# Performance work log

Hardware: AMD Instinct MI355X
Metric: run time of the kernel (lower is better)

The kernel has to match this reference:

```python
import jax, jax.numpy as jnp
import numpy as np

N_QUBITS = 6
N_QLAYERS = 3
LOGISTIC_R = 3.99
HENON_A, HENON_B = 1.4, 0.3


def _conv1d(x, w, b):
    # x: [B, C_in, T], w: [C_out, C_in, K=3], SAME padding (pad=1)
    y = jax.lax.conv_general_dilated(x, w, window_strides=(1,), padding=((1, 1),),
                                     dimension_numbers=('NCH', 'OIH', 'NCH'))
    return y + b[None, :, None]


def _apply_1q_batched(state, G, q):
    # state: [B,2,...,2], G: [B,2,2] acting on qubit axis 1+q
    s = jnp.moveaxis(state, 1 + q, -1)
    s = jnp.einsum('bij,b...j->b...i', G, s)
    return jnp.moveaxis(s, -1, 1 + q)


def _apply_1q(state, G, q):
    s = jnp.moveaxis(state, 1 + q, -1)
    s = jnp.einsum('ij,b...j->b...i', G, s)
    return jnp.moveaxis(s, -1, 1 + q)


def _apply_cnot(state, c, t):
    s = jnp.moveaxis(state, (1 + c, 1 + t), (-2, -1))
    # control=1 block: flip target amplitudes
    s = jnp.concatenate([s[..., 0:1, :], s[..., 1:2, ::-1]], axis=-2)
    return jnp.moveaxis(s, (-2, -1), (1 + c, 1 + t))


def quantum_expvals(angles, qweights):
    # angles: [B, 6] real encoding angles; qweights: [3, 6] shared RY params
    B = angles.shape[0]
    state = jnp.zeros((B, 2 ** N_QUBITS), jnp.complex64).at[:, 0].set(1.0)
    state = state.reshape((B,) + (2,) * N_QUBITS)
    half = 0.5 * angles
    for i in range(N_QUBITS):
        ax = half[:, i % N_QUBITS]
        ay = half[:, (i + 1) % N_QUBITS]
        az = half[:, (i + 2) % N_QUBITS]
        cx_, sx_ = jnp.cos(ax), jnp.sin(ax)
        RX = jnp.stack([jnp.stack([cx_ + 0j, -1j * sx_], -1),
                        jnp.stack([-1j * sx_, cx_ + 0j], -1)], -2)
        state = _apply_1q_batched(state, RX, i)
        cy_, sy_ = jnp.cos(ay), jnp.sin(ay)
        RY = jnp.stack([jnp.stack([cy_ + 0j, -sy_ + 0j], -1),
                        jnp.stack([sy_ + 0j, cy_ + 0j], -1)], -2)
        state = _apply_1q_batched(state, RY, i)
        ez = jnp.exp(1j * az)
        zero = jnp.zeros_like(ez)
        RZ = jnp.stack([jnp.stack([jnp.conj(ez), zero], -1),
                        jnp.stack([zero, ez], -1)], -2)
        state = _apply_1q_batched(state, RZ, i)
    for l in range(N_QLAYERS):
        for q in range(N_QUBITS):
            a = 0.5 * qweights[l, q]
            c_, s_ = jnp.cos(a), jnp.sin(a)
            RY = jnp.array([[1., 0.], [0., 1.]], jnp.float32) * c_ + \
                 jnp.array([[0., -1.], [1., 0.]], jnp.float32) * s_
            state = _apply_1q(state, RY.astype(jnp.complex64), q)
        for q in range(N_QUBITS):
            state = _apply_cnot(state, q, (q + 1) % N_QUBITS)
    probs = (state * jnp.conj(state)).real  # [B,2,...,2]
    evs = []
    for i in range(N_QUBITS):
        axes = tuple(a for a in range(1, N_QUBITS + 1) if a != 1 + i)
        p = jnp.sum(probs, axis=axes)  # [B,2]
        evs.append(p[:, 0] - p[:, 1])
    return jnp.stack(evs, -1)  # [B,6]


def _lstm_cell(xt, h, c, Wih, Whh, bih, bhh):
    g = xt @ Wih.T + bih + h @ Whh.T + bhh
    i, f, gg, o = jnp.split(g, 4, axis=-1)
    c2 = jax.nn.sigmoid(f) * c + jax.nn.sigmoid(i) * jnp.tanh(gg)
    h2 = jax.nn.sigmoid(o) * jnp.tanh(c2)
    return h2, c2


def _forward(x, w0, b0, w1, b1, w2, b2, Wih, Whh, bih, bhh, qweights, Wfc, bfc, Wout, bout):
    B = x.shape[0]
    t = x.transpose(0, 2, 1)                 # [B, C, T]
    t = jax.nn.relu(_conv1d(t, w0, b0))
    t = jax.nn.relu(_conv1d(t, w1, b1))
    t = jax.nn.relu(_conv1d(t, w2, b2))
    t = t.transpose(2, 0, 1)                 # [T, B, H]
    H = t.shape[2]
    h0 = jnp.zeros((B, H), x.dtype)
    c0 = jnp.zeros((B, H), x.dtype)

    def step(carry, xt):
        h, c = carry
        h, c = _lstm_cell(xt, h, c, Wih, Whh, bih, bhh)
        h = LOGISTIC_R * h * (1.0 - h)
        x0, y0 = h[:, 0], h[:, 1]
        xn = 1.0 - HENON_A * x0 ** 2 + y0
        yn = HENON_B * x0
        h = jnp.concatenate([xn[:, None], yn[:, None], h[:, 2:]], axis=1)
        # QuantumRNNCell called as qrnn(hx, hx): h = h + fc(quantum(h[:, :6]))
        h = h + quantum_expvals(h[:, :N_QUBITS], qweights) @ Wfc.T + bfc
        return (h, c), None

    (h, _), _ = jax.lax.scan(step, (h0, c0), t)
    return jax.nn.sigmoid(h @ Wout.T + bout)  # [B, 1]


def setup_inputs() -> dict:
    key = jax.random.key(0)
    ks = jax.random.split(key, 20)
    B, T, D, Htcn, Hlstm = 1024, 256, 64, 32, 32
    s = 0.1
    inp = {
        'x': jax.random.normal(ks[0], (B, T, D), jnp.float32),
        'w0': jax.random.normal(ks[1], (Htcn, D, 3), jnp.float32) * s,
        'b0': jax.random.normal(ks[2], (Htcn,), jnp.float32) * s,
        'w1': jax.random.normal(ks[3], (Htcn, Htcn, 3), jnp.float32) * s,
        'b1': jax.random.normal(ks[4], (Htcn,), jnp.float32) * s,
        'w2': jax.random.normal(ks[5], (Htcn, Htcn, 3), jnp.float32) * s,
        'b2': jax.random.normal(ks[6], (Htcn,), jnp.float32) * s,
        'Wih': jax.random.normal(ks[7], (4 * Hlstm, Htcn), jnp.float32) * s,
        'Whh': jax.random.normal(ks[8], (4 * Hlstm, Hlstm), jnp.float32) * s,
        'bih': jax.random.normal(ks[9], (4 * Hlstm,), jnp.float32) * s,
        'bhh': jax.random.normal(ks[10], (4 * Hlstm,), jnp.float32) * s,
        'qweights': jax.random.normal(ks[11], (N_QLAYERS, N_QUBITS), jnp.float32),
        'Wfc': jax.random.normal(ks[12], (Hlstm, N_QUBITS), jnp.float32) * s,
        'bfc': jax.random.normal(ks[13], (Hlstm,), jnp.float32) * s,
        'Wout': jax.random.normal(ks[14], (1, Hlstm), jnp.float32) * s,
        'bout': jax.random.normal(ks[15], (1,), jnp.float32) * s,
    }
    return inp


def reference(x, w0, b0, w1, b1, w2, b2, Wih, Whh, bih, bhh, qweights, Wfc, bfc, Wout, bout):
    return _forward(x, w0, b0, w1, b1, w2, b2, Wih, Whh, bih, bhh, qweights, Wfc, bfc, Wout, bout)
```

## Files before the change

kernel.cpp:

```cpp
#include <hip/hip_runtime.h>

#define B_SIZE 1024
#define T_LEN  256
#define D_IN   64
#define HC     32

typedef int   v2i_t __attribute__((ext_vector_type(2)));
typedef float v2f   __attribute__((ext_vector_type(2)));

__device__ __forceinline__ float frcp(float x){ return __builtin_amdgcn_rcpf(x); }
__device__ __forceinline__ float rfl(float x){
    return __uint_as_float(__builtin_amdgcn_readfirstlane(__float_as_uint(x)));
}
__device__ __forceinline__ float rdlane(float x, int l){
    return __int_as_float(__builtin_amdgcn_readlane(__float_as_int(x), l));
}
__device__ __forceinline__ float ftanh(float x){
    return 1.f - 2.f*frcp(__expf(2.f*x) + 1.f);
}
__device__ __forceinline__ float fsigmoid(float x){
    return frcp(1.f + __expf(-x));
}

template<int CTRL>
__device__ __forceinline__ int dppmov(int x){
    return __builtin_amdgcn_update_dpp(x, x, CTRL, 0xF, 0xF, false);
}

template<int M>
__device__ __forceinline__ int dpp_xor(int x){
    static_assert(M >= 1 && M <= 15, "dpp_xor mask");
    constexpr int hi = M & 12;
    constexpr int q  = (hi == 4 || hi == 12) ? ((M & 3) ^ 3) : (M & 3);
    if constexpr (q == 1) x = dppmov<0xB1>(x);
    else if constexpr (q == 2) x = dppmov<0x4E>(x);
    else if constexpr (q == 3) x = dppmov<0x1B>(x);
    if constexpr (hi == 4)       x = dppmov<0x141>(x);
    else if constexpr (hi == 8)  x = dppmov<0x128>(x);
    else if constexpr (hi == 12) x = dppmov<0x140>(x);
    return x;
}

#if defined(__has_builtin)
#  if __has_builtin(__builtin_amdgcn_permlane16_swap)
#    define HAVE_PL16 1
#  endif
#endif

template<int M>
__device__ __forceinline__ float xshuf(float xf){
    if constexpr (M == 0) return xf;
    int x = __float_as_int(xf);
    if constexpr (M & 15) x = dpp_xor<M & 15>(x);
    if constexpr (M & 16){
#ifdef HAVE_PL16
        v2i_t r = __builtin_amdgcn_permlane16_swap(x, x, false, false);
        x = r.x ^ r.y ^ x;
#else
        x = __builtin_amdgcn_ds_swizzle(x, (16 << 10) | 0x1F);
#endif
    }
    if constexpr (M & 32){
        v2i_t r = __builtin_amdgcn_permlane32_swap(x, x, false, false);
        x = r.x ^ r.y ^ x;
    }
    return __int_as_float(x);
}

struct QMasks { int M[3][6]; int S[3][6]; int R[6]; };
constexpr QMasks qmasks(){
    QMasks qm{};
    unsigned m[6], n[6];
    for (int i = 0; i < 6; i++){ m[i] = 1u << i; n[i] = 1u << i; }
    for (int l = 0; l < 3; l++){
        for (int q = 0; q < 6; q++){
            unsigned u = m[q], r = 0;
            for (int i = 0; i < 6; i++) if ((u >> i) & 1u) r |= (32u >> i);
            qm.S[l][q] = (int)r;
            unsigned u2 = 0;
            for (int i = 0; i < 6; i++) u2 |= ((n[i] >> q) & 1u) << i;
            unsigned r2 = 0;
            for (int i = 0; i < 6; i++) if ((u2 >> i) & 1u) r2 |= (32u >> i);
            qm.M[l][q] = (int)r2;
        }
        for (int q = 0; q < 6; q++) m[(q + 1) % 6] ^= m[q];
        n[0] ^= n[5];
        for (int q = 4; q >= 0; q--) n[q + 1] ^= n[q];
    }
    for (int i = 0; i < 6; i++){
        unsigned u = m[i], r = 0;
        for (int j = 0; j < 6; j++) if ((u >> j) & 1u) r |= (32u >> j);
        qm.R[i] = (int)r;
    }
    return qm;
}
constexpr QMasks QM = qmasks();

__global__ __launch_bounds__(256) void conv0_kernel(const float* __restrict__ x,
    const float* __restrict__ w0, const float* __restrict__ b0, float* __restrict__ out)
{
    __shared__ __align__(16) float xs[130*65];
    __shared__ __align__(16) float wl[192*36];
    const int tid = threadIdx.x;
    const int b  = blockIdx.x >> 1;
    const int s0 = (blockIdx.x & 1) * 128;

    for (int idx = tid; idx < 130*64; idx += 256){
        int r = idx >> 6, d = idx & 63;
        int s = s0 - 1 + r;
        float v = 0.f;
        if (s >= 0 && s < T_LEN) v = x[(size_t)b*(T_LEN*D_IN) + (size_t)s*D_IN + d];
        xs[r*65 + d] = v;
    }
    for (int idx = tid; idx < 192*32; idx += 256){
        int c = idx / 192, r = idx - c*192;
        wl[r*36 + c] = w0[idx];
    }
    __syncthreads();

    const int c0 = (tid & 7) * 4;
    const int sl = (tid >> 3) * 4;
    float acc[4][4];
    #pragma unroll
    for (int ci = 0; ci < 4; ci++){
        float bb = b0[c0+ci];
        #pragma unroll
        for (int m = 0; m < 4; m++) acc[ci][m] = bb;
    }
    for (int d = 0; d < 64; d++){
        float xv[6];
        #pragma unroll
        for (int o = 0; o < 6; o++) xv[o] = xs[(sl+o)*65 + d];
        #pragma unroll
        for (int kk = 0; kk < 3; kk++){
            const float4 wv = *(const float4*)&wl[(d*3+kk)*36 + c0];
            float w4[4] = {wv.x, wv.y, wv.z, wv.w};
            #pragma unroll
            for (int ci = 0; ci < 4; ci++)
                #pragma unroll
                for (int m = 0; m < 4; m++)
                    acc[ci][m] += xv[m+kk]*w4[ci];
        }
    }
    #pragma unroll
    for (int ci = 0; ci < 4; ci++){
        float4 v;
        v.x = fmaxf(acc[ci][0], 0.f); v.y = fmaxf(acc[ci][1], 0.f);
        v.z = fmaxf(acc[ci][2], 0.f); v.w = fmaxf(acc[ci][3], 0.f);
        *(float4*)&out[(size_t)b*(HC*T_LEN) + (size_t)(c0+ci)*T_LEN + (s0+sl)] = v;
    }
}

template<bool TOUT>
__global__ __launch_bounds__(256) void convm_kernel(const float* __restrict__ in,
    const float* __restrict__ w, const float* __restrict__ bias, float* __restrict__ out)
{
    __shared__ __align__(16) float xs[130*33];
    __shared__ __align__(16) float wl[96*36];
    const int tid = threadIdx.x;
    const int b  = blockIdx.x >> 1;
    const int s0 = (blockIdx.x & 1) * 128;

    for (int idx = tid; idx < 32*130; idx += 256){
        int ci = idx / 130; int r = idx - ci*130;
        int s = s0 - 1 + r;
        float v = 0.f;
        if (s >= 0 && s < T_LEN) v = in[(size_t)b*(HC*T_LEN) + (size_t)ci*T_LEN + s];
        xs[r*33 + ci] = v;
    }
    for (int idx = tid; idx < 96*32; idx += 256){
        int c = idx / 96, r = idx - c*96;
        wl[r*36 + c] = w[idx];
    }
    __syncthreads();

    const int c0 = (tid & 7) * 4;
    const int sl = (tid >> 3) * 4;
    float acc[4][4];
    #pragma unroll
    for (int ci = 0; ci < 4; ci++){
        float bb = bias[c0+ci];
        #pragma unroll
        for (int m = 0; m < 4; m++) acc[ci][m] = bb;
    }
    for (int ci2 = 0; ci2 < 32; ci2++){
        float xv[6];
        #pragma unroll
        for (int o = 0; o < 6; o++) xv[o] = xs[(sl+o)*33 + ci2];
        #pragma unroll
        for (int kk = 0; kk < 3; kk++){
            const float4 wv = *(const float4*)&wl[(ci2*3+kk)*36 + c0];
            float w4[4] = {wv.x, wv.y, wv.z, wv.w};
            #pragma unroll
            for (int ci = 0; ci < 4; ci++)
                #pragma unroll
                for (int m = 0; m < 4; m++)
                    acc[ci][m] += xv[m+kk]*w4[ci];
        }
    }
    if (!TOUT){
        #pragma unroll
        for (int ci = 0; ci < 4; ci++){
            float4 v;
            v.x = fmaxf(acc[ci][0], 0.f); v.y = fmaxf(acc[ci][1], 0.f);
            v.z = fmaxf(acc[ci][2], 0.f); v.w = fmaxf(acc[ci][3], 0.f);
            *(float4*)&out[(size_t)b*(HC*T_LEN) + (size_t)(c0+ci)*T_LEN + (s0+sl)] = v;
        }
    } else {
        #pragma unroll
        for (int m = 0; m < 4; m++){
            int s = s0 + sl + m;
            float4 v;
            v.x = fmaxf(acc[0][m], 0.f); v.y = fmaxf(acc[1][m], 0.f);
            v.z = fmaxf(acc[2][m], 0.f); v.w = fmaxf(acc[3][m], 0.f);
            *(float4*)&out[(size_t)s*(B_SIZE*HC) + (size_t)b*HC + c0] = v;
        }
    }
}

__global__ __launch_bounds__(256) void convm_gates_kernel(const float* __restrict__ in,
    const float* __restrict__ w, const float* __restrict__ bias,
    const float* __restrict__ Wih, const float* __restrict__ bih,
    const float* __restrict__ bhh, float* __restrict__ G)
{
    __shared__ __align__(16) float smem[4292 + 3456];
    float* xs = smem;
    float* wl = smem + 4292;
    float* ts = smem;
    const int tid = threadIdx.x;
    const int b  = blockIdx.x >> 1;
    const int s0 = (blockIdx.x & 1) * 128;

    for (int idx = tid; idx < 32*130; idx += 256){
        int ci = idx / 130; int r = idx - ci*130;
        int s = s0 - 1 + r;
        float v = 0.f;
        if (s >= 0 && s < T_LEN) v = in[(size_t)b*(HC*T_LEN) + (size_t)ci*T_LEN + s];
        xs[r*33 + ci] = v;
    }
    for (int idx = tid; idx < 96*32; idx += 256){
        int c = idx / 96, r = idx - c*96;
        wl[r*36 + c] = w[idx];
    }
    __syncthreads();

    const int c0 = (tid & 7) * 4;
    const int sl = (tid >> 3) * 4;
    float acc[4][4];
    #pragma unroll
    for (int ci = 0; ci < 4; ci++){
        float bb = bias[c0+ci];
        #pragma unroll
        for (int m = 0; m < 4; m++) acc[ci][m] = bb;
    }
    for (int ci2 = 0; ci2 < 32; ci2++){
        float xv[6];
        #pragma unroll
        for (int o = 0; o < 6; o++) xv[o] = xs[(sl+o)*33 + ci2];
        #pragma unroll
        for (int kk = 0; kk < 3; kk++){
            const float4 wv = *(const float4*)&wl[(ci2*3+kk)*36 + c0];
            float w4[4] = {wv.x, wv.y, wv.z, wv.w};
            #pragma unroll
            for (int ci = 0; ci < 4; ci++)
                #pragma unroll
                for (int m = 0; m < 4; m++)
                    acc[ci][m] += xv[m+kk]*w4[ci];
        }
    }
    __syncthreads();

    #pragma unroll
    for (int m = 0; m < 4; m++){
        float4 v;
        v.x = fmaxf(acc[0][m], 0.f); v.y = fmaxf(acc[1][m], 0.f);
        v.z = fmaxf(acc[2][m], 0.f); v.w = fmaxf(acc[3][m], 0.f);
        *(float4*)&ts[(sl+m)*36 + c0] = v;
    }
    __syncthreads();

    const int r = tid & 127;
    const int half = tid >> 7;
    float4 wr[8];
    #pragma unroll
    for (int j4 = 0; j4 < 8; j4++) wr[j4] = ((const float4*)Wih)[r*8 + j4];
    const float br = bih[r] + bhh[r];

    for (int ss = half; ss < 128; ss += 2){
        float a0 = br, a1 = 0.f, a2 = 0.f, a3 = 0.f;
        #pragma unroll
        for (int j4 = 0; j4 < 8; j4++){
            const float4 xv = *(const float4*)&ts[ss*36 + j4*4];
            a0 += wr[j4].x*xv.x; a1 += wr[j4].y*xv.y;
            a2 += wr[j4].z*xv.z; a3 += wr[j4].w*xv.w;
        }
        G[((size_t)(s0+ss)*B_SIZE + b)*128 + r] = (a0+a1)+(a2+a3);
    }
}

__global__ __launch_bounds__(256, 1) void scan_kernel(
    const float* __restrict__ G,   const float* __restrict__ Whh,
    const float* __restrict__ qw,  const float* __restrict__ Wfc,
    const float* __restrict__ bfc, const float* __restrict__ Wout,
    const float* __restrict__ bout, float* __restrict__ out)
{
    const unsigned lane = threadIdx.x & 63u;
    const int wv   = threadIdx.x >> 6;
    const int b    = __builtin_amdgcn_readfirstlane(blockIdx.x * 4 + wv);
    const int r1 = lane, r2 = lane + 64;
    const int k  = lane & 31;

    v2f uAB[32];
    #pragma unroll
    for (int j4 = 0; j4 < 8; j4++){
        float4 d_ = ((const float4*)Whh)[r1*8 + j4];
        float4 e  = ((const float4*)Whh)[r2*8 + j4];
        uAB[j4*4+0] = v2f{d_.x, e.x}; uAB[j4*4+1] = v2f{d_.y, e.y};
        uAB[j4*4+2] = v2f{d_.z, e.z}; uAB[j4*4+3] = v2f{d_.w, e.w};
    }

    float wfcr[6];
    #pragma unroll
    for (int j = 0; j < 6; j++) wfcr[j] = Wfc[k*6 + j];
    const float bfcl  = bfc[k];
    const float woutl = (lane < 32) ? Wout[k] : 0.f;
    const float boutv = bout[0];

    float cgv[18], ssin[18];
    #pragma unroll
    for (int g = 0; g < 18; g++){
        int l = g / 6, q = g % 6;
        float a = 0.5f * qw[g];
        float cv = __cosf(a), sv = __sinf(a);
        cgv[g] = rfl(cv);
        unsigned sm = (unsigned)QM.S[l][q];
        ssin[g] = (__builtin_popcount(sm & lane) & 1) ? sv : -sv;
    }
    float wsgn[6];
    #pragma unroll
    for (int j = 0; j < 6; j++) wsgn[j] = (lane & (1u << j)) ? -1.f : 1.f;
    const bool qs[6] = { (lane & 32u) != 0, (lane & 16u) != 0, (lane & 8u) != 0,
                         (lane & 4u) != 0,  (lane & 2u) != 0,  (lane & 1u) != 0 };

    float h = 0.f, c = 0.f;
    const float* gbase = G + (size_t)b*128;
    float g1 = gbase[r1], g2 = gbase[r2];

    #pragma clang loop unroll(disable)
    for (int s = 0; s < T_LEN; s++){
        const float cg1 = g1, cg2 = g2;
        {
            int s2 = (s + 1 < T_LEN) ? s + 1 : s;
            const float* gn = gbase + (size_t)s2*(B_SIZE*128);
            g1 = gn[r1]; g2 = gn[r2];
        }

        v2f a0 = v2f{cg1, cg2}, a1 = v2f{0.f,0.f}, a2 = v2f{0.f,0.f}, a3 = v2f{0.f,0.f};
        #pragma unroll
        for (int j = 0; j < 32; j += 4){
            float h0 = rdlane(h, j),   h1 = rdlane(h, j+1);
            float h2 = rdlane(h, j+2), h3 = rdlane(h, j+3);
            a0 += h0*uAB[j]; a1 += h1*uAB[j+1]; a2 += h2*uAB[j+2]; a3 += h3*uAB[j+3];
        }
        v2f accv = (a0+a1)+(a2+a3);
        float acc1 = accv.x, acc2 = accv.y;

        float sigA = fsigmoid(acc1);
        float argB = (lane < 32) ? acc2 : 0.5f*acc2;
        float tt   = ftanh(argB);
        float actB = (lane < 32) ? tt : (0.5f + 0.5f*tt);
        float fsig = xshuf<32>(sigA);
        float osig = xshuf<32>(actB);
        c = fsig*c + sigA*actB;
        float hn = osig * ftanh(c);

        hn = 3.99f * hn * (1.f - hn);
        float x0 = rdlane(hn, 0), y0 = rdlane(hn, 1);
        float xnv = 1.f - 1.4f*x0*x0 + y0;
        float ynv = 0.3f * x0;

        float ang[6];
        ang[0] = 0.5f*xnv; ang[1] = 0.5f*ynv;
        ang[2] = 0.5f*rdlane(hn, 2); ang[3] = 0.5f*rdlane(hn, 3);
        ang[4] = 0.5f*rdlane(hn, 4); ang[5] = 0.5f*rdlane(hn, 5);
        float ca[6], sa[6];
        #pragma unroll
        for (int j = 0; j < 6; j++){ ca[j] = __cosf(ang[j]); sa[j] = __sinf(ang[j]); }

        float fr[6], fi[6];
        #pragma unroll
        for (int i = 0; i < 6; i++){
            const int i1 = (i+1)%6, i2 = (i+2)%6;
            float cx=ca[i], sx=sa[i], cy=ca[i1], sy=sa[i1], cz=ca[i2], sz=sa[i2];
            float w0r = cy*cx, w0i = sy*sx;
            float w1r = sy*cx, w1i = -cy*sx;
            float q0r = cz*w0r + sz*w0i, q0i = cz*w0i - sz*w0r;
            float q1r = cz*w1r - sz*w1i, q1i = cz*w1i + sz*w1r;
            fr[i] = qs[i] ? q1r : q0r;
            fi[i] = qs[i] ? q1i : q0i;
        }
        v2f t01 = v2f{fr[0]*fr[1] - fi[0]*fi[1], fr[0]*fi[1] + fi[0]*fr[1]};
        v2f t23 = v2f{fr[2]*fr[3] - fi[2]*fi[3], fr[2]*fi[3] + fi[2]*fr[3]};
        v2f t45 = v2f{fr[4]*fr[5] - fi[4]*fi[5], fr[4]*fi[5] + fi[4]*fr[5]};
        v2f t03 = v2f{t01.x*t23.x - t01.y*t23.y, t01.x*t23.y + t01.y*t23.x};
        v2f av  = v2f{t03.x*t45.x - t03.y*t45.y, t03.x*t45.y + t03.y*t45.x};

        #define GATE(L,Q) { \
            constexpr int MM = QM.M[L][Q]; \
            v2f bv; bv.x = xshuf<MM>(av.x); bv.y = xshuf<MM>(av.y); \
            av = cgv[(L)*6+(Q)]*av + ssin[(L)*6+(Q)]*bv; }
        GATE(0,0) GATE(0,1) GATE(0,2) GATE(0,3) GATE(0,4) GATE(0,5)
        GATE(1,0) GATE(1,1) GATE(1,2) GATE(1,3) GATE(1,4) GATE(1,5)
        GATE(2,0) GATE(2,1) GATE(2,2) GATE(2,3) GATE(2,4) GATE(2,5)
        #undef GATE

        float wp = av.x*av.x + av.y*av.y;
        wp = wsgn[0]*wp + xshuf< 1>(wp);
        wp = wsgn[1]*wp + xshuf< 2>(wp);
        wp = wsgn[2]*wp + xshuf< 4>(wp);
        wp = wsgn[3]*wp + xshuf< 8>(wp);
        wp = wsgn[4]*wp + xshuf<16>(wp);
        wp = wsgn[5]*wp + xshuf<32>(wp);
        float ev0 = rdlane(wp, QM.R[0]), ev1 = rdlane(wp, QM.R[1]);
        float ev2 = rdlane(wp, QM.R[2]), ev3 = rdlane(wp, QM.R[3]);
        float ev4 = rdlane(wp, QM.R[4]), ev5 = rdlane(wp, QM.R[5]);

        float upd = bfcl + (wfcr[0]*ev0 + wfcr[1]*ev1)
                         + (wfcr[2]*ev2 + wfcr[3]*ev3)
                         + (wfcr[4]*ev4 + wfcr[5]*ev5);

        float hsel = hn;
        hsel = (lane == 0u) ? xnv : hsel;
        hsel = (lane == 1u) ? ynv : hsel;
        h = hsel + upd;
    }

    float pv = (lane < 32) ? h*woutl : 0.f;
    #pragma unroll
    for (int off = 32; off; off >>= 1) pv += __shfl_xor(pv, off, 64);
    if (lane == 0) out[b] = fsigmoid(pv + boutv);
}

__global__ __launch_bounds__(256, 1) void scan_legacy(
    const float* __restrict__ tS,
    const float* __restrict__ Wih, const float* __restrict__ Whh,
    const float* __restrict__ bih, const float* __restrict__ bhh,
    const float* __restrict__ qw,  const float* __restrict__ Wfc,
    const float* __restrict__ bfc, const float* __restrict__ Wout,
    const float* __restrict__ bout, float* __restrict__ out)
{
    const unsigned lane = threadIdx.x & 63u;
    const int wv   = threadIdx.x >> 6;
    const int b    = __builtin_amdgcn_readfirstlane(blockIdx.x * 4 + wv);
    const int r1 = lane, r2 = lane + 64;
    const int k  = lane & 31;

    float wA[32], wB[32], uA[32], uB[32];
    #pragma unroll
    for (int j4 = 0; j4 < 8; j4++){
        float4 a  = ((const float4*)Wih)[r1*8 + j4];
        float4 c_ = ((const float4*)Wih)[r2*8 + j4];
        float4 d_ = ((const float4*)Whh)[r1*8 + j4];
        float4 e  = ((const float4*)Whh)[r2*8 + j4];
        wA[j4*4+0]=a.x;  wA[j4*4+1]=a.y;  wA[j4*4+2]=a.z;  wA[j4*4+3]=a.w;
        wB[j4*4+0]=c_.x; wB[j4*4+1]=c_.y; wB[j4*4+2]=c_.z; wB[j4*4+3]=c_.w;
        uA[j4*4+0]=d_.x; uA[j4*4+1]=d_.y; uA[j4*4+2]=d_.z; uA[j4*4+3]=d_.w;
        uB[j4*4+0]=e.x;  uB[j4*4+1]=e.y;  uB[j4*4+2]=e.z;  uB[j4*4+3]=e.w;
    }
    const float bias1 = bih[r1] + bhh[r1];
    const float bias2 = bih[r2] + bhh[r2];

    float wfcr[6];
    #pragma unroll
    for (int j = 0; j < 6; j++) wfcr[j] = Wfc[k*6 + j];
    const float bfcl  = bfc[k];
    const float woutl = (lane < 32) ? Wout[k] : 0.f;
    const float boutv = bout[0];

    float cgv[18], ssin[18];
    #pragma unroll
    for (int g = 0; g < 18; g++){
        int l = g / 6, q = g % 6;
        float a = 0.5f * qw[g];
        float cv = __cosf(a), sv = __sinf(a);
        cgv[g] = rfl(cv);
        unsigned sm = (unsigned)QM.S[l][q];
        ssin[g] = (__builtin_popcount(sm & lane) & 1) ? sv : -sv;
    }
    float wsgn[6];
    #pragma unroll
    for (int j = 0; j < 6; j++) wsgn[j] = (lane & (1u << j)) ? -1.f : 1.f;
    const bool qs[6] = { (lane & 32u) != 0, (lane & 16u) != 0, (lane & 8u) != 0,
                         (lane & 4u) != 0,  (lane & 2u) != 0,  (lane & 1u) != 0 };

    float h = 0.f, c = 0.f;
    const float* xbase = tS + (size_t)b * HC;

    float4 xf[8];
    #pragma unroll
    for (int j4 = 0; j4 < 8; j4++) xf[j4] = ((const float4*)xbase)[j4];

    #pragma clang loop unroll(disable)
    for (int s = 0; s < T_LEN; s++){
        float xt[32];
        #pragma unroll
        for (int j4 = 0; j4 < 8; j4++){
            xt[j4*4+0]=xf[j4].x; xt[j4*4+1]=xf[j4].y; xt[j4*4+2]=xf[j4].z; xt[j4*4+3]=xf[j4].w;
        }
        {
            int s2 = (s + 1 < T_LEN) ? s + 1 : s;
            const float4* np_ = (const float4*)(xbase + (size_t)s2*(B_SIZE*HC));
            #pragma unroll
            for (int j4 = 0; j4 < 8; j4++) xf[j4] = np_[j4];
        }

        float a1a = bias1, a1b = 0.f, a2a = bias2, a2b = 0.f;
        #pragma unroll
        for (int j = 0; j < 32; j += 2){
            a1a += xt[j]*wA[j];     a1b += xt[j+1]*wA[j+1];
            a2a += xt[j]*wB[j];     a2b += xt[j+1]*wB[j+1];
        }
        #pragma unroll
        for (int j = 0; j < 32; j += 2){
            float h0 = rdlane(h, j), h1 = rdlane(h, j+1);
            a1a += h0*uA[j];   a1b += h1*uA[j+1];
            a2a += h0*uB[j];   a2b += h1*uB[j+1];
        }
        float acc1 = a1a + a1b, acc2 = a2a + a2b;

        float sigA = fsigmoid(acc1);
        float argB = (lane < 32) ? acc2 : 0.5f*acc2;
        float tt   = ftanh(argB);
        float actB = (lane < 32) ? tt : (0.5f + 0.5f*tt);
        float fsig = xshuf<32>(sigA);
        float osig = xshuf<32>(actB);
        c = fsig*c + sigA*actB;
        float hn = osig * ftanh(c);

        hn = 3.99f * hn * (1.f - hn);
        float x0 = rdlane(hn, 0), y0 = rdlane(hn, 1);
        float xnv = 1.f - 1.4f*x0*x0 + y0;
        float ynv = 0.3f * x0;

        float ang[6];
        ang[0] = 0.5f*xnv; ang[1] = 0.5f*ynv;
        ang[2] = 0.5f*rdlane(hn, 2); ang[3] = 0.5f*rdlane(hn, 3);
        ang[4] = 0.5f*rdlane(hn, 4); ang[5] = 0.5f*rdlane(hn, 5);
        float ca[6], sa[6];
        #pragma unroll
        for (int j = 0; j < 6; j++){ ca[j] = __cosf(ang[j]); sa[j] = __sinf(ang[j]); }

        float fr[6], fi[6];
        #pragma unroll
        for (int i = 0; i < 6; i++){
            const int i1 = (i+1)%6, i2 = (i+2)%6;
            float cx=ca[i], sx=sa[i], cy=ca[i1], sy=sa[i1], cz=ca[i2], sz=sa[i2];
            float w0r = cy*cx, w0i = sy*sx;
            float w1r = sy*cx, w1i = -cy*sx;
            float q0r = cz*w0r + sz*w0i, q0i = cz*w0i - sz*w0r;
            float q1r = cz*w1r - sz*w1i, q1i = cz*w1i + sz*w1r;
            fr[i] = qs[i] ? q1r : q0r;
            fi[i] = qs[i] ? q1i : q0i;
        }
        float t01r = fr[0]*fr[1] - fi[0]*fi[1], t01i = fr[0]*fi[1] + fi[0]*fr[1];
        float t23r = fr[2]*fr[3] - fi[2]*fi[3], t23i = fr[2]*fi[3] + fi[2]*fr[3];
        float t45r = fr[4]*fr[5] - fi[4]*fi[5], t45i = fr[4]*fi[5] + fi[4]*fr[5];
        float t03r = t01r*t23r - t01i*t23i,     t03i = t01r*t23i + t01i*t23r;
        float ar   = t03r*t45r - t03i*t45i,     ai   = t03r*t45i + t03i*t45r;

        #define GATE(L,Q) { \
            constexpr int MM = QM.M[L][Q]; \
            float br = xshuf<MM>(ar), bi = xshuf<MM>(ai); \
            float cg = cgv[(L)*6+(Q)], ss = ssin[(L)*6+(Q)]; \
            ar = cg*ar + ss*br; ai = cg*ai + ss*bi; }
        GATE(0,0) GATE(0,1) GATE(0,2) GATE(0,3) GATE(0,4) GATE(0,5)
        GATE(1,0) GATE(1,1) GATE(1,2) GATE(1,3) GATE(1,4) GATE(1,5)
        GATE(2,0) GATE(2,1) GATE(2,2) GATE(2,3) GATE(2,4) GATE(2,5)
        #undef GATE

        float wp = ar*ar + ai*ai;
        wp = wsgn[0]*wp + xshuf< 1>(wp);
        wp = wsgn[1]*wp + xshuf< 2>(wp);
        wp = wsgn[2]*wp + xshuf< 4>(wp);
        wp = wsgn[3]*wp + xshuf< 8>(wp);
        wp = wsgn[4]*wp + xshuf<16>(wp);
        wp = wsgn[5]*wp + xshuf<32>(wp);
        float ev0 = rdlane(wp, QM.R[0]), ev1 = rdlane(wp, QM.R[1]);
        float ev2 = rdlane(wp, QM.R[2]), ev3 = rdlane(wp, QM.R[3]);
        float ev4 = rdlane(wp, QM.R[4]), ev5 = rdlane(wp, QM.R[5]);

        float upd = bfcl + (wfcr[0]*ev0 + wfcr[1]*ev1)
                         + (wfcr[2]*ev2 + wfcr[3]*ev3)
                         + (wfcr[4]*ev4 + wfcr[5]*ev5);

        float hsel = hn;
        hsel = (lane == 0u) ? xnv : hsel;
        hsel = (lane == 1u) ? ynv : hsel;
        h = hsel + upd;
    }

    float pv = (lane < 32) ? h*woutl : 0.f;
    #pragma unroll
    for (int off = 32; off; off >>= 1) pv += __shfl_xor(pv, off, 64);
    if (lane == 0) out[b] = fsigmoid(pv + boutv);
}

extern "C" void kernel_launch(void* const* d_in, const int* in_sizes, int n_in,
                              void* d_out, int out_size, void* d_ws, size_t ws_size,
                              hipStream_t stream)
{
    (void)in_sizes; (void)n_in; (void)out_size;
    const float* x    = (const float*)d_in[0];
    const float* w0   = (const float*)d_in[1];
    const float* b0   = (const float*)d_in[2];
    const float* w1   = (const float*)d_in[3];
    const float* b1   = (const float*)d_in[4];
    const float* w2   = (const float*)d_in[5];
    const float* b2   = (const float*)d_in[6];
    const float* Wih  = (const float*)d_in[7];
    const float* Whh  = (const float*)d_in[8];
    const float* bih  = (const float*)d_in[9];
    const float* bhh  = (const float*)d_in[10];
    const float* qw   = (const float*)d_in[11];
    const float* Wfc  = (const float*)d_in[12];
    const float* bfc  = (const float*)d_in[13];
    const float* Wout = (const float*)d_in[14];
    const float* bout = (const float*)d_in[15];
    float* out = (float*)d_out;

    const size_t tensorN = (size_t)B_SIZE*HC*T_LEN;
    float* t0 = (float*)d_ws;
    float* t1 = t0 + tensorN;
    float* G  = t1 + tensorN;
    const size_t need = (2*tensorN + (size_t)T_LEN*B_SIZE*128) * sizeof(float);

    conv0_kernel<<<2048, 256, 0, stream>>>(x, w0, b0, t0);
    convm_kernel<false><<<2048, 256, 0, stream>>>(t0, w1, b1, t1);
    if (ws_size >= need){
        convm_gates_kernel<<<2048, 256, 0, stream>>>(t1, w2, b2, Wih, bih, bhh, G);
        scan_kernel<<<256, 256, 0, stream>>>(G, Whh, qw, Wfc, bfc, Wout, bout, out);
    } else {
        float* tS = t0;
        convm_kernel<true ><<<2048, 256, 0, stream>>>(t1, w2, b2, tS);
        scan_legacy<<<256, 256, 0, stream>>>(tS, Wih, Whh, bih, bhh, qw, Wfc, bfc, Wout, bout, out);
    }
}
```

Before: 660.4 us.

## Fuse conv1, conv2 and input-gate projection into one kernel with halo recompute

Merges the second and third conv layers with the LSTM input-gate GEMM into a single kernel. conv1 is recomputed over a two-sample halo in shared memory, so the t1 intermediate never goes to global memory and one launch is removed. conv0 now stages its input in two 32-channel halves to shrink shared memory and raise occupancy. The gate stage computes two gate rows per thread. The cost is redundant halo rows of conv1, uneven per-thread work, and extra barriers.

```diff
diff --git a/kernel.cpp b/kernel.cpp
--- a/kernel.cpp
+++ b/kernel.cpp
@@ -99,24 +99,16 @@
 __global__ __launch_bounds__(256) void conv0_kernel(const float* __restrict__ x,
     const float* __restrict__ w0, const float* __restrict__ b0, float* __restrict__ out)
 {
-    __shared__ __align__(16) float xs[130*65];
+    __shared__ float xs[130*33];
     __shared__ __align__(16) float wl[192*36];
     const int tid = threadIdx.x;
     const int b  = blockIdx.x >> 1;
     const int s0 = (blockIdx.x & 1) * 128;
 
-    for (int idx = tid; idx < 130*64; idx += 256){
-        int r = idx >> 6, d = idx & 63;
-        int s = s0 - 1 + r;
-        float v = 0.f;
-        if (s >= 0 && s < T_LEN) v = x[(size_t)b*(T_LEN*D_IN) + (size_t)s*D_IN + d];
-        xs[r*65 + d] = v;
-    }
     for (int idx = tid; idx < 192*32; idx += 256){
         int c = idx / 192, r = idx - c*192;
         wl[r*36 + c] = w0[idx];
     }
-    __syncthreads();
 
     const int c0 = (tid & 7) * 4;
     const int sl = (tid >> 3) * 4;
@@ -127,19 +119,32 @@
         #pragma unroll
         for (int m = 0; m < 4; m++) acc[ci][m] = bb;
     }
-    for (int d = 0; d < 64; d++){
-        float xv[6];
-        #pragma unroll
-        for (int o = 0; o < 6; o++) xv[o] = xs[(sl+o)*65 + d];
-        #pragma unroll
-        for (int kk = 0; kk < 3; kk++){
-            const float4 wv = *(const float4*)&wl[(d*3+kk)*36 + c0];
-            float w4[4] = {wv.x, wv.y, wv.z, wv.w};
-            #pragma unroll
-            for (int ci = 0; ci < 4; ci++)
+
+    for (int half = 0; half < 2; half++){
+        __syncthreads();
+        for (int idx = tid; idx < 130*32; idx += 256){
+            int r = idx >> 5, d = idx & 31;
+            int s = s0 - 1 + r;
+            float v = 0.f;
+            if (s >= 0 && s < T_LEN) v = x[(size_t)b*(T_LEN*D_IN) + (size_t)s*D_IN + half*32 + d];
+            xs[r*33 + d] = v;
+        }
+        __syncthreads();
+        for (int d = 0; d < 32; d++){
+            float xv[6];
+            #pragma unroll
+            for (int o = 0; o < 6; o++) xv[o] = xs[(sl+o)*33 + d];
+            const int dd = half*32 + d;
+            #pragma unroll
+            for (int kk = 0; kk < 3; kk++){
+                const float4 wv = *(const float4*)&wl[(dd*3+kk)*36 + c0];
+                float w4[4] = {wv.x, wv.y, wv.z, wv.w};
                 #pragma unroll
-                for (int m = 0; m < 4; m++)
-                    acc[ci][m] += xv[m+kk]*w4[ci];
+                for (int ci = 0; ci < 4; ci++)
+                    #pragma unroll
+                    for (int m = 0; m < 4; m++)
+                        acc[ci][m] += xv[m+kk]*w4[ci];
+            }
         }
     }
     #pragma unroll
@@ -148,6 +153,144 @@
         v.x = fmaxf(acc[ci][0], 0.f); v.y = fmaxf(acc[ci][1], 0.f);
         v.z = fmaxf(acc[ci][2], 0.f); v.w = fmaxf(acc[ci][3], 0.f);
         *(float4*)&out[(size_t)b*(HC*T_LEN) + (size_t)(c0+ci)*T_LEN + (s0+sl)] = v;
+    }
+}
+
+__global__ __launch_bounds__(256) void conv12g_kernel(const float* __restrict__ t0g,
+    const float* __restrict__ w1, const float* __restrict__ b1,
+    const float* __restrict__ w2, const float* __restrict__ b2,
+    const float* __restrict__ Wih, const float* __restrict__ bih,
+    const float* __restrict__ bhh, float* __restrict__ G)
+{
+    __shared__ __align__(16) float smem[4608 + 3456 + 4290];
+    float* t0t = smem;
+    float* t2t = smem;
+    float* wlr = smem + 4608;
+    float* t1t = smem + 4608 + 3456;
+    const int tid = threadIdx.x;
+    const int b  = blockIdx.x >> 1;
+    const int s0 = (blockIdx.x & 1) * 128;
+
+    for (int idx = tid; idx < 132*32; idx += 256){
+        int ci = idx / 132, r = idx - ci*132;
+        int s = s0 - 2 + r;
+        float v = 0.f;
+        if (s >= 0 && s < T_LEN) v = t0g[(size_t)b*(HC*T_LEN) + (size_t)ci*T_LEN + s];
+        t0t[r*33 + ci] = v;
+    }
+    for (int idx = tid; idx < 96*32; idx += 256){
+        int c = idx / 96, r = idx - c*96;
+        wlr[r*36 + c] = w1[idx];
+    }
+    __syncthreads();
+
+    const int c0 = (tid & 7) * 4;
+    const int g  = tid >> 3;
+    const int base1 = (g < 30) ? 4*g : (120 + 5*(g - 30));
+    const int nr1   = (g < 30) ? 4 : 5;
+    {
+        float acc[4][5];
+        #pragma unroll
+        for (int ci = 0; ci < 4; ci++){
+            float bb = b1[c0+ci];
+            #pragma unroll
+            for (int m = 0; m < 5; m++) acc[ci][m] = bb;
+        }
+        for (int ci2 = 0; ci2 < 32; ci2++){
+            float xv[7];
+            #pragma unroll
+            for (int o = 0; o < 7; o++) xv[o] = t0t[(base1+o)*33 + ci2];
+            #pragma unroll
+            for (int kk = 0; kk < 3; kk++){
+                const float4 wv = *(const float4*)&wlr[(ci2*3+kk)*36 + c0];
+                float w4[4] = {wv.x, wv.y, wv.z, wv.w};
+                #pragma unroll
+                for (int ci = 0; ci < 4; ci++)
+                    #pragma unroll
+                    for (int m = 0; m < 5; m++)
+                        acc[ci][m] += xv[m+kk]*w4[ci];
+            }
+        }
+        #pragma unroll
+        for (int m = 0; m < 5; m++){
+            if (m < nr1){
+                const int rt = base1 + m;
+                const int s_act = s0 - 1 + rt;
+                const bool inb = (s_act >= 0) && (s_act < T_LEN);
+                #pragma unroll
+                for (int ci = 0; ci < 4; ci++)
+                    t1t[rt*33 + c0 + ci] = inb ? fmaxf(acc[ci][m], 0.f) : 0.f;
+            }
+        }
+    }
+    __syncthreads();
+
+    for (int idx = tid; idx < 96*32; idx += 256){
+        int c = idx / 96, r = idx - c*96;
+        wlr[r*36 + c] = w2[idx];
+    }
+    __syncthreads();
+
+    const int base2 = 4*g;
+    {
+        float acc[4][4];
+        #pragma unroll
+        for (int ci = 0; ci < 4; ci++){
+            float bb = b2[c0+ci];
+            #pragma unroll
+            for (int m = 0; m < 4; m++) acc[ci][m] = bb;
+        }
+        for (int ci2 = 0; ci2 < 32; ci2++){
+            float xv[6];
+            #pragma unroll
+            for (int o = 0; o < 6; o++) xv[o] = t1t[(base2+o)*33 + ci2];
+            #pragma unroll
+            for (int kk = 0; kk < 3; kk++){
+                const float4 wv = *(const float4*)&wlr[(ci2*3+kk)*36 + c0];
+                float w4[4] = {wv.x, wv.y, wv.z, wv.w};
+                #pragma unroll
+                for (int ci = 0; ci < 4; ci++)
+                    #pragma unroll
+                    for (int m = 0; m < 4; m++)
+                        acc[ci][m] += xv[m+kk]*w4[ci];
+            }
+        }
+        __syncthreads();
+        #pragma unroll
+        for (int m = 0; m < 4; m++){
+            float4 v;
+            v.x = fmaxf(acc[0][m], 0.f); v.y = fmaxf(acc[1][m], 0.f);
+            v.z = fmaxf(acc[2][m], 0.f); v.w = fmaxf(acc[3][m], 0.f);
+            *(float4*)&t2t[(base2+m)*36 + c0] = v;
+        }
+    }
+    __syncthreads();
+
+    const int r = tid & 63;
+    const int wvv = tid >> 6;
+    float4 wrA[8], wrB[8];
+    #pragma unroll
+    for (int j4 = 0; j4 < 8; j4++){
+        wrA[j4] = ((const float4*)Wih)[r*8 + j4];
+        wrB[j4] = ((const float4*)Wih)[(r+64)*8 + j4];
+    }
+    const float brA = bih[r]    + bhh[r];
+    const float brB = bih[r+64] + bhh[r+64];
+
+    for (int ss = wvv; ss < 128; ss += 4){
+        float a0 = brA, a1 = 0.f, a2 = 0.f, a3 = 0.f;
+        float e0 = brB, e1 = 0.f, e2 = 0.f, e3 = 0.f;
+        #pragma unroll
+        for (int j4 = 0; j4 < 8; j4++){
+            const float4 xv = *(const float4*)&t2t[ss*36 + j4*4];
+            a0 += wrA[j4].x*xv.x; a1 += wrA[j4].y*xv.y;
+            a2 += wrA[j4].z*xv.z; a3 += wrA[j4].w*xv.w;
+            e0 += wrB[j4].x*xv.x; e1 += wrB[j4].y*xv.y;
+            e2 += wrB[j4].z*xv.z; e3 += wrB[j4].w*xv.w;
+        }
+        const size_t gi = ((size_t)(s0+ss)*B_SIZE + b)*128 + r;
+        G[gi]      = (a0+a1)+(a2+a3);
+        G[gi + 64] = (e0+e1)+(e2+e3);
     }
 }
 
@@ -215,86 +358,6 @@
             v.z = fmaxf(acc[2][m], 0.f); v.w = fmaxf(acc[3][m], 0.f);
             *(float4*)&out[(size_t)s*(B_SIZE*HC) + (size_t)b*HC + c0] = v;
         }
-    }
-}
-
-__global__ __launch_bounds__(256) void convm_gates_kernel(const float* __restrict__ in,
-    const float* __restrict__ w, const float* __restrict__ bias,
-    const float* __restrict__ Wih, const float* __restrict__ bih,
-    const float* __restrict__ bhh, float* __restrict__ G)
-{
-    __shared__ __align__(16) float smem[4292 + 3456];
-    float* xs = smem;
-    float* wl = smem + 4292;
-    float* ts = smem;
-    const int tid = threadIdx.x;
-    const int b  = blockIdx.x >> 1;
-    const int s0 = (blockIdx.x & 1) * 128;
-
-    for (int idx = tid; idx < 32*130; idx += 256){
-        int ci = idx / 130; int r = idx - ci*130;
-        int s = s0 - 1 + r;
-        float v = 0.f;
-        if (s >= 0 && s < T_LEN) v = in[(size_t)b*(HC*T_LEN) + (size_t)ci*T_LEN + s];
-        xs[r*33 + ci] = v;
-    }
-    for (int idx = tid; idx < 96*32; idx += 256){
-        int c = idx / 96, r = idx - c*96;
-        wl[r*36 + c] = w[idx];
-    }
-    __syncthreads();
-
-    const int c0 = (tid & 7) * 4;
-    const int sl = (tid >> 3) * 4;
-    float acc[4][4];
-    #pragma unroll
-    for (int ci = 0; ci < 4; ci++){
-        float bb = bias[c0+ci];
-        #pragma unroll
-        for (int m = 0; m < 4; m++) acc[ci][m] = bb;
-    }
-    for (int ci2 = 0; ci2 < 32; ci2++){
-        float xv[6];
-        #pragma unroll
-        for (int o = 0; o < 6; o++) xv[o] = xs[(sl+o)*33 + ci2];
-        #pragma unroll
-        for (int kk = 0; kk < 3; kk++){
-            const float4 wv = *(const float4*)&wl[(ci2*3+kk)*36 + c0];
-            float w4[4] = {wv.x, wv.y, wv.z, wv.w};
-            #pragma unroll
-            for (int ci = 0; ci < 4; ci++)
-                #pragma unroll
-                for (int m = 0; m < 4; m++)
-                    acc[ci][m] += xv[m+kk]*w4[ci];
-        }
-    }
-    __syncthreads();
-
-    #pragma unroll
-    for (int m = 0; m < 4; m++){
-        float4 v;
-        v.x = fmaxf(acc[0][m], 0.f); v.y = fmaxf(acc[1][m], 0.f);
-        v.z = fmaxf(acc[2][m], 0.f); v.w = fmaxf(acc[3][m], 0.f);
-        *(float4*)&ts[(sl+m)*36 + c0] = v;
-    }
-    __syncthreads();
-
-    const int r = tid & 127;
-    const int half = tid >> 7;
-    float4 wr[8];
-    #pragma unroll
-    for (int j4 = 0; j4 < 8; j4++) wr[j4] = ((const float4*)Wih)[r*8 + j4];
-    const float br = bih[r] + bhh[r];
-
-    for (int ss = half; ss < 128; ss += 2){
-        float a0 = br, a1 = 0.f, a2 = 0.f, a3 = 0.f;
-        #pragma unroll
-        for (int j4 = 0; j4 < 8; j4++){
-            const float4 xv = *(const float4*)&ts[ss*36 + j4*4];
-            a0 += wr[j4].x*xv.x; a1 += wr[j4].y*xv.y;
-            a2 += wr[j4].z*xv.z; a3 += wr[j4].w*xv.w;
-        }
-        G[((size_t)(s0+ss)*B_SIZE + b)*128 + r] = (a0+a1)+(a2+a3);
     }
 }
 
@@ -630,17 +693,17 @@
 
     const size_t tensorN = (size_t)B_SIZE*HC*T_LEN;
     float* t0 = (float*)d_ws;
-    float* t1 = t0 + tensorN;
-    float* G  = t1 + tensorN;
-    const size_t need = (2*tensorN + (size_t)T_LEN*B_SIZE*128) * sizeof(float);
+    float* G  = t0 + tensorN;
+    const size_t need = (tensorN + (size_t)T_LEN*B_SIZE*128) * sizeof(float);
 
     conv0_kernel<<<2048, 256, 0, stream>>>(x, w0, b0, t0);
-    convm_kernel<false><<<2048, 256, 0, stream>>>(t0, w1, b1, t1);
     if (ws_size >= need){
-        convm_gates_kernel<<<2048, 256, 0, stream>>>(t1, w2, b2, Wih, bih, bhh, G);
+        conv12g_kernel<<<2048, 256, 0, stream>>>(t0, w1, b1, w2, b2, Wih, bih, bhh, G);
         scan_kernel<<<256, 256, 0, stream>>>(G, Whh, qw, Wfc, bfc, Wout, bout, out);
     } else {
+        float* t1 = t0 + tensorN;
         float* tS = t0;
+        convm_kernel<false><<<2048, 256, 0, stream>>>(t0, w1, b1, t1);
         convm_kernel<true ><<<2048, 256, 0, stream>>>(t1, w2, b2, tS);
         scan_legacy<<<256, 256, 0, stream>>>(tS, Wih, Whh, bih, bhh, qw, Wfc, bfc, Wout, bout, out);
     }
```

Measured after the change: 636.6 us. -3.6%, faster.
